# Kernel optimization log

Hardware: AMD Instinct MI355X
Metric: run time of the kernel (lower is better)

Reference implementation:

```python
import jax, jax.numpy as jnp
import numpy as np

GRID_SIZE = 5
SPLINE_ORDER = 3
GRID_LO, GRID_HI = -3.0, 3.0
B, IN_DIM, UNITS, SUB_DIM, NSUB = 4096, 512, 1024, 512, 3


def make_grid(in_features):
    h = (GRID_HI - GRID_LO) / GRID_SIZE
    g = jnp.arange(-SPLINE_ORDER, GRID_SIZE + SPLINE_ORDER + 1, dtype=jnp.float32) * h + GRID_LO
    return jnp.broadcast_to(g, (in_features, g.shape[0]))  # (in, 12)


def b_splines(x, grid):
    # x: (..., in), grid: (in, G) -> (..., in, grid_size + spline_order)
    x = x[..., None]
    bases = ((x >= grid[:, :-1]) & (x < grid[:, 1:])).astype(x.dtype)
    for k in range(1, SPLINE_ORDER + 1):
        left = (x - grid[:, :-(k + 1)]) / (grid[:, k:-1] - grid[:, :-(k + 1)])
        right = (grid[:, k + 1:] - x) / (grid[:, k + 1:] - grid[:, 1:-k])
        bases = left * bases[..., :-1] + right * bases[..., 1:]
    return bases


def setup_inputs() -> dict:
    key = jax.random.key(0)
    ks = jax.random.split(key, 16)
    sw = lambda k, shape, scale: jax.random.normal(k, shape, dtype=jnp.float32) * scale
    inp = {
        'x': sw(ks[0], (B, IN_DIM), 1.0),
        'h0': sw(ks[1], (B, UNITS), 0.1),
        'c0': sw(ks[2], (B, UNITS), 0.1),
        'sub_states': sw(ks[3], (NSUB, B, SUB_DIM), 0.1),
        'kernel': sw(ks[4], (IN_DIM, UNITS * 3), 1.0 / np.sqrt(IN_DIM)),
        'recurrent_kernel': sw(ks[5], (UNITS, UNITS * 3), 1.0 / np.sqrt(UNITS)),
        'bias': jnp.zeros((UNITS * 3,), jnp.float32).at[UNITS:2 * UNITS].set(1.0),
        'sub_kernel_inputs': sw(ks[6], (NSUB, IN_DIM, SUB_DIM), 1.0 / np.sqrt(IN_DIM)),
        'sub_kernel_states': sw(ks[7], (NSUB, SUB_DIM, SUB_DIM), 1.0 / np.sqrt(SUB_DIM)),
        'sub_recurrent_kernel': sw(ks[8], (NSUB, SUB_DIM * 2), 0.5),
        'base_weight': sw(ks[9], (NSUB, SUB_DIM, SUB_DIM), 1.0 / np.sqrt(SUB_DIM)),
        'spline_weight': sw(ks[10], (NSUB, SUB_DIM, SUB_DIM, GRID_SIZE + SPLINE_ORDER), 0.02),
        'spline_scaler': sw(ks[11], (NSUB, SUB_DIM, SUB_DIM), 1.0),
        'aggregated_weight': sw(ks[12], (NSUB * SUB_DIM, UNITS), 1.0 / np.sqrt(NSUB * SUB_DIM)),
        'aggregated_bias': jnp.zeros((UNITS,), jnp.float32),
    }
    return inp


def reference(x, h0, c0, sub_states, kernel, recurrent_kernel, bias,
              sub_kernel_inputs, sub_kernel_states, sub_recurrent_kernel,
              base_weight, spline_weight, spline_scaler,
              aggregated_weight, aggregated_bias):
    grid = make_grid(SUB_DIM)

    # LSTM-style gates: gates = sigmoid(x@W + h@U + b)
    z = x @ kernel + h0 @ recurrent_kernel + bias
    g = jax.nn.sigmoid(z)
    i, f, c_gate = jnp.split(g, 3, axis=-1)
    c_new = f * c0 + i * jnp.tanh(c_gate)

    # Sub-layer inputs: agg[k] = x @ Wx[k] + sub_state[k] @ Wh[k]  -> (k, b, sub_in)
    agg = (jnp.einsum('bi,kis->kbs', x, sub_kernel_inputs)
           + jnp.einsum('kbo,kos->kbs', sub_states, sub_kernel_states))

    # KANLinear: base branch + spline branch (stacked over k sub-layers)
    base_out = jnp.einsum('kbs,kos->kbo', jax.nn.silu(agg), base_weight)
    bases = b_splines(agg, grid)                         # (k, b, sub_in, 8)
    scaled_sw = spline_weight * spline_scaler[..., None]  # (k, out, in, 8)
    spline_out = jnp.einsum('kbic,koic->kbo', bases, scaled_sw)
    sub_out = base_out + spline_out                       # (k, b, sub_out)

    # Recurrent sub-state update
    rk_h = sub_recurrent_kernel[:, None, :SUB_DIM]
    rk_x = sub_recurrent_kernel[:, None, SUB_DIM:]
    new_sub_states = rk_h * sub_out + rk_x * sub_states

    # Output gate from aggregated sub-layer outputs
    agg_flat = jnp.transpose(sub_out, (1, 0, 2)).reshape(x.shape[0], NSUB * SUB_DIM)
    o = jax.nn.sigmoid(agg_flat @ aggregated_weight + aggregated_bias)
    h_new = o * jnp.tanh(c_new)
    return h_new, c_new, new_sub_states
```

## Files before the change

kernel.cpp:

```cpp
#include <hip/hip_runtime.h>

#define B_DIM   4096
#define INF     512
#define UNITS_  1024
#define SUBD    512
#define NSUB_   3
#define NBAS    8
#define G3K     (SUBD * NBAS)

typedef __attribute__((ext_vector_type(8))) short bf16x8_t;
typedef __attribute__((ext_vector_type(4))) float f32x4_t;
typedef unsigned short u16;

__device__ __forceinline__ u16 f2bf(float f) {
    union { float f; unsigned int u; } v; v.f = f;
    unsigned int r = v.u + 0x7fffu + ((v.u >> 16) & 1u);
    return (u16)(r >> 16);
}
__device__ __forceinline__ float bf2f(u16 h) {
    union { unsigned int u; float f; } v; v.u = ((unsigned int)h) << 16;
    return v.f;
}
__device__ __forceinline__ float sigm(float x) { return 1.0f / (1.0f + __expf(-x)); }
__device__ __forceinline__ float tanh_(float x) {
    float e = __expf(2.0f * x);
    return 1.0f - 2.0f / (e + 1.0f);
}

__device__ __forceinline__ void gload_lds16(const void* g, void* l) {
    __builtin_amdgcn_global_load_lds(
        (const __attribute__((address_space(1))) unsigned int*)g,
        (__attribute__((address_space(3))) unsigned int*)l, 16, 0, 0);
}

__global__ void k_f32_to_bf16(const float* __restrict__ in, u16* __restrict__ out, int n4) {
    int i = blockIdx.x * blockDim.x + threadIdx.x;
    if (i >= n4) return;
    float4 v = ((const float4*)in)[i];
    ushort4 r; r.x = f2bf(v.x); r.y = f2bf(v.y); r.z = f2bf(v.z); r.w = f2bf(v.w);
    ((ushort4*)out)[i] = r;
}

__global__ void k_ssw(const float* __restrict__ sw, const float* __restrict__ sc,
                      u16* __restrict__ out, int n4) {
    int i = blockIdx.x * blockDim.x + threadIdx.x;
    if (i >= n4) return;
    float4 v = ((const float4*)sw)[i];
    float s = sc[i >> 1];
    ushort4 r; r.x = f2bf(v.x * s); r.y = f2bf(v.y * s); r.z = f2bf(v.z * s); r.w = f2bf(v.w * s);
    ((ushort4*)out)[i] = r;
}

__global__ void k_tconv(const float* __restrict__ in, u16* __restrict__ out,
                        int R, int C, size_t inStride, size_t outStride) {
    in  += (size_t)blockIdx.z * inStride;
    out += (size_t)blockIdx.z * outStride;
    __shared__ float tile[32][33];
    int c0 = blockIdx.x * 32, r0 = blockIdx.y * 32;
    int tx = threadIdx.x, ty = threadIdx.y;
#pragma unroll
    for (int j = 0; j < 4; ++j)
        tile[ty + j * 8][tx] = in[(size_t)(r0 + ty + j * 8) * C + c0 + tx];
    __syncthreads();
#pragma unroll
    for (int j = 0; j < 4; ++j)
        out[(size_t)(c0 + ty + j * 8) * R + r0 + tx] = f2bf(tile[tx][ty + j * 8]);
}

__global__ void k_cnew(const u16* __restrict__ gbuf, const float* __restrict__ c0,
                       float* __restrict__ c_out, int n4) {
    int i = blockIdx.x * blockDim.x + threadIdx.x;
    if (i >= n4) return;
    int u4 = i * 4;
    int b = u4 >> 10, u = u4 & 1023;
    const u16* gr = gbuf + (size_t)b * 3072 + u;
    ushort4 gi = *(const ushort4*)gr;
    ushort4 gf = *(const ushort4*)(gr + 1024);
    ushort4 gc = *(const ushort4*)(gr + 2048);
    float4 c0v = ((const float4*)c0)[i];
    float4 r;
    r.x = bf2f(gf.x) * c0v.x + bf2f(gi.x) * tanh_(bf2f(gc.x));
    r.y = bf2f(gf.y) * c0v.y + bf2f(gi.y) * tanh_(bf2f(gc.y));
    r.z = bf2f(gf.z) * c0v.z + bf2f(gi.z) * tanh_(bf2f(gc.z));
    r.w = bf2f(gf.w) * c0v.w + bf2f(gi.w) * tanh_(bf2f(gc.w));
    ((float4*)c_out)[i] = r;
}

__global__ void k_bases(const float* __restrict__ agg, u16* __restrict__ bases,
                        u16* __restrict__ silu, int n) {
    for (int i = blockIdx.x * blockDim.x + threadIdx.x; i < n; i += gridDim.x * blockDim.x) {
        float x = agg[i];
        silu[i] = f2bf(x * sigm(x));
        float b[11];
#pragma unroll
        for (int j = 0; j < 11; ++j) {
            float tj  = 1.2f * (float)(j - 3) - 3.0f;
            float tj1 = 1.2f * (float)(j - 2) - 3.0f;
            b[j] = (x >= tj && x < tj1) ? 1.0f : 0.0f;
        }
#pragma unroll
        for (int k = 1; k <= 3; ++k) {
            float inv = 1.0f / (1.2f * (float)k);
#pragma unroll
            for (int j = 0; j < 11; ++j) {
                if (j > 10 - k) break;
                float tj   = 1.2f * (float)(j - 3) - 3.0f;
                float tjk1 = 1.2f * (float)(j + k - 2) - 3.0f;
                b[j] = (x - tj) * inv * b[j] + (tjk1 - x) * inv * b[j + 1];
            }
        }
        bf16x8_t v;
#pragma unroll
        for (int j = 0; j < 8; ++j) v[j] = (short)f2bf(b[j]);
        *(bf16x8_t*)(bases + (size_t)i * 8) = v;
    }
}

struct Seg { const u16* A; const u16* B; int ldA; int ldB; int nkt; };

template<int NS>
__device__ __forceinline__ void gemm_core(const Seg segs[NS], int rowBase, int colBase,
                                          u16* ldsA, u16* ldsB, f32x4_t acc[4][4]) {
    const int t = threadIdx.x;
    const int lane = t & 63, wave = t >> 6;
    const int wR = (wave >> 1) * 64, wC = (wave & 1) * 64;
    const int l15 = lane & 15, lk = (lane >> 4) * 8;
    const int sr = lane >> 3;
    const int scol = (lane & 7) * 8;
#pragma unroll
    for (int s = 0; s < NS; ++s) {
        const u16* Ag = segs[s].A + (size_t)rowBase * segs[s].ldA;
        const u16* Bg = segs[s].B + (size_t)colBase * segs[s].ldB;
        const int ldA = segs[s].ldA, ldB = segs[s].ldB, nkt = segs[s].nkt;
        for (int kt = 0; kt < nkt; ++kt) {
            __syncthreads();
#pragma unroll
            for (int i = 0; i < 4; ++i) {
                int ci = wave * 4 + i;
                int r = ci * 8 + sr;
                gload_lds16(Ag + (size_t)r * ldA + kt * 64 + scol, ldsA + ci * 512);
                gload_lds16(Bg + (size_t)r * ldB + kt * 64 + scol, ldsB + ci * 512);
            }
            __syncthreads();
#pragma unroll
            for (int kk = 0; kk < 2; ++kk) {
                bf16x8_t a[4], b[4];
#pragma unroll
                for (int m = 0; m < 4; ++m)
                    a[m] = *(const bf16x8_t*)(ldsA + (wR + m * 16 + l15) * 64 + kk * 32 + lk);
#pragma unroll
                for (int n = 0; n < 4; ++n)
                    b[n] = *(const bf16x8_t*)(ldsB + (wC + n * 16 + l15) * 64 + kk * 32 + lk);
#pragma unroll
                for (int m = 0; m < 4; ++m)
#pragma unroll
                    for (int n = 0; n < 4; ++n)
                        acc[m][n] = __builtin_amdgcn_mfma_f32_16x16x32_bf16(a[m], b[n], acc[m][n], 0, 0, 0);
            }
        }
    }
}

#define GEMM_PRE()                                                         \
    __shared__ u16 ldsA[128 * 64], ldsB[128 * 64];                         \
    int rowBase = blockIdx.y * 128, colBase = blockIdx.x * 128;            \
    f32x4_t acc[4][4];                                                     \
    _Pragma("unroll") for (int m = 0; m < 4; ++m)                          \
        _Pragma("unroll") for (int n = 0; n < 4; ++n)                      \
            acc[m][n] = (f32x4_t){0.f, 0.f, 0.f, 0.f};

#define EPI_IDX()                                                          \
    const int lane = threadIdx.x & 63, wave = threadIdx.x >> 6;            \
    const int wR = (wave >> 1) * 64, wC = (wave & 1) * 64;                 \
    const int l15 = lane & 15, r4 = (lane >> 4) * 4;

__global__ __launch_bounds__(256) void k_gemm1(const u16* xb, const u16* h0b,
                                               const u16* kT, const u16* rkT,
                                               const float* __restrict__ bias,
                                               u16* __restrict__ gbuf) {
    GEMM_PRE();
    Seg segs[2] = { { xb, kT, INF, INF, INF / 64 },
                    { h0b, rkT, UNITS_, UNITS_, UNITS_ / 64 } };
    gemm_core<2>(segs, rowBase, colBase, ldsA, ldsB, acc);
    EPI_IDX();
#pragma unroll
    for (int m = 0; m < 4; ++m)
#pragma unroll
        for (int n = 0; n < 4; ++n)
#pragma unroll
            for (int j = 0; j < 4; ++j) {
                int row = rowBase + wR + m * 16 + r4 + j;
                int col = colBase + wC + n * 16 + l15;
                gbuf[(size_t)row * 3072 + col] = f2bf(sigm(acc[m][n][j] + bias[col]));
            }
}

__global__ __launch_bounds__(256) void k_gemm2(const u16* xb, const u16* ssb,
                                               const u16* skiT, const u16* sksT,
                                               float* __restrict__ agg) {
    GEMM_PRE();
    int k = blockIdx.z;
    Seg segs[2] = { { xb, skiT + (size_t)k * SUBD * INF, INF, INF, INF / 64 },
                    { ssb + (size_t)k * B_DIM * SUBD, sksT + (size_t)k * SUBD * SUBD, SUBD, SUBD, SUBD / 64 } };
    gemm_core<2>(segs, rowBase, colBase, ldsA, ldsB, acc);
    EPI_IDX();
#pragma unroll
    for (int m = 0; m < 4; ++m)
#pragma unroll
        for (int n = 0; n < 4; ++n)
#pragma unroll
            for (int j = 0; j < 4; ++j) {
                int row = rowBase + wR + m * 16 + r4 + j;
                int col = colBase + wC + n * 16 + l15;
                agg[((size_t)k * B_DIM + row) * SUBD + col] = acc[m][n][j];
            }
}

__global__ __launch_bounds__(256) void k_gemm3(const u16* silu, const u16* bases,
                                               const u16* bwb, const u16* sswb,
                                               const float* __restrict__ srk,
                                               const float* __restrict__ ss,
                                               float* __restrict__ nss_out,
                                               u16* __restrict__ subfl) {
    GEMM_PRE();
    int k = blockIdx.z;
    Seg segs[2] = { { silu + (size_t)k * B_DIM * SUBD, bwb + (size_t)k * SUBD * SUBD, SUBD, SUBD, SUBD / 64 },
                    { bases + (size_t)k * B_DIM * G3K, sswb + (size_t)k * SUBD * G3K, G3K, G3K, G3K / 64 } };
    gemm_core<2>(segs, rowBase, colBase, ldsA, ldsB, acc);
    EPI_IDX();
#pragma unroll
    for (int m = 0; m < 4; ++m)
#pragma unroll
        for (int n = 0; n < 4; ++n)
#pragma unroll
            for (int j = 0; j < 4; ++j) {
                int row = rowBase + wR + m * 16 + r4 + j;
                int col = colBase + wC + n * 16 + l15;
                float so = acc[m][n][j];
                float rh = srk[k * 1024 + col];
                float rx = srk[k * 1024 + 512 + col];
                size_t o = ((size_t)k * B_DIM + row) * SUBD + col;
                nss_out[o] = rh * so + rx * ss[o];
                subfl[(size_t)row * 1536 + k * SUBD + col] = f2bf(so);
            }
}

__global__ __launch_bounds__(256) void k_gemm4(const u16* subfl, const u16* awT,
                                               const float* __restrict__ abias,
                                               const float* __restrict__ c_new,
                                               float* __restrict__ h_out) {
    GEMM_PRE();
    Seg segs[1] = { { subfl, awT, 1536, 1536, 1536 / 64 } };
    gemm_core<1>(segs, rowBase, colBase, ldsA, ldsB, acc);
    EPI_IDX();
#pragma unroll
    for (int m = 0; m < 4; ++m)
#pragma unroll
        for (int n = 0; n < 4; ++n)
#pragma unroll
            for (int j = 0; j < 4; ++j) {
                int row = rowBase + wR + m * 16 + r4 + j;
                int col = colBase + wC + n * 16 + l15;
                float ov = sigm(acc[m][n][j] + abias[col]);
                h_out[(size_t)row * 1024 + col] = ov * tanh_(c_new[(size_t)row * 1024 + col]);
            }
}

extern "C" void kernel_launch(void* const* d_in, const int* in_sizes, int n_in,
                              void* d_out, int out_size, void* d_ws, size_t ws_size,
                              hipStream_t stream) {
    const float* x    = (const float*)d_in[0];
    const float* h0   = (const float*)d_in[1];
    const float* c0   = (const float*)d_in[2];
    const float* ss   = (const float*)d_in[3];
    const float* Wk   = (const float*)d_in[4];
    const float* Wr   = (const float*)d_in[5];
    const float* bias = (const float*)d_in[6];
    const float* ski  = (const float*)d_in[7];
    const float* sks  = (const float*)d_in[8];
    const float* srk  = (const float*)d_in[9];
    const float* bw   = (const float*)d_in[10];
    const float* sw   = (const float*)d_in[11];
    const float* sc   = (const float*)d_in[12];
    const float* aw   = (const float*)d_in[13];
    const float* ab   = (const float*)d_in[14];

    float* out_h   = (float*)d_out;
    float* out_c   = out_h + (size_t)B_DIM * UNITS_;
    float* out_nss = out_c + (size_t)B_DIM * UNITS_;

    char* w = (char*)d_ws;
    auto take = [&](size_t bytes) -> char* {
        char* p = w; w += (bytes + 255) & ~(size_t)255; return p;
    };
    u16*   xb    = (u16*)take((size_t)B_DIM * INF * 2);
    u16*   h0b   = (u16*)take((size_t)B_DIM * UNITS_ * 2);
    u16*   ssb   = (u16*)take((size_t)NSUB_ * B_DIM * SUBD * 2);
    u16*   kT    = (u16*)take((size_t)3072 * INF * 2);
    u16*   rkT   = (u16*)take((size_t)3072 * UNITS_ * 2);
    u16*   skiT  = (u16*)take((size_t)NSUB_ * SUBD * INF * 2);
    u16*   sksT  = (u16*)take((size_t)NSUB_ * SUBD * SUBD * 2);
    u16*   bwb   = (u16*)take((size_t)NSUB_ * SUBD * SUBD * 2);
    u16*   sswb  = (u16*)take((size_t)NSUB_ * SUBD * G3K * 2);
    u16*   awT   = (u16*)take((size_t)UNITS_ * 1536 * 2);
    float* agg   = (float*)take((size_t)NSUB_ * B_DIM * SUBD * 4);
    u16*   siluB = (u16*)take((size_t)NSUB_ * B_DIM * SUBD * 2);
    u16*   subfl = (u16*)take((size_t)B_DIM * 1536 * 2);
    u16*   basesB= (u16*)take((size_t)NSUB_ * B_DIM * G3K * 2);
    u16*   gbuf  = basesB;

    dim3 tb(256);
    k_f32_to_bf16<<<(B_DIM * INF / 4 + 255) / 256, tb, 0, stream>>>(x, xb, B_DIM * INF / 4);
    k_f32_to_bf16<<<(B_DIM * UNITS_ / 4 + 255) / 256, tb, 0, stream>>>(h0, h0b, B_DIM * UNITS_ / 4);
    k_f32_to_bf16<<<(NSUB_ * B_DIM * SUBD / 4 + 255) / 256, tb, 0, stream>>>(ss, ssb, NSUB_ * B_DIM * SUBD / 4);
    k_f32_to_bf16<<<(NSUB_ * SUBD * SUBD / 4 + 255) / 256, tb, 0, stream>>>(bw, bwb, NSUB_ * SUBD * SUBD / 4);
    k_ssw<<<(NSUB_ * SUBD * G3K / 4 + 255) / 256, tb, 0, stream>>>(sw, sc, sswb, NSUB_ * SUBD * G3K / 4);
    dim3 tt(32, 8);
    k_tconv<<<dim3(3072 / 32, INF / 32, 1), tt, 0, stream>>>(Wk, kT, INF, 3072, 0, 0);
    k_tconv<<<dim3(3072 / 32, UNITS_ / 32, 1), tt, 0, stream>>>(Wr, rkT, UNITS_, 3072, 0, 0);
    k_tconv<<<dim3(SUBD / 32, INF / 32, NSUB_), tt, 0, stream>>>(ski, skiT, INF, SUBD,
                                                                 (size_t)INF * SUBD, (size_t)SUBD * INF);
    k_tconv<<<dim3(SUBD / 32, SUBD / 32, NSUB_), tt, 0, stream>>>(sks, sksT, SUBD, SUBD,
                                                                  (size_t)SUBD * SUBD, (size_t)SUBD * SUBD);
    k_tconv<<<dim3(UNITS_ / 32, 1536 / 32, 1), tt, 0, stream>>>(aw, awT, 1536, UNITS_, 0, 0);

    k_gemm1<<<dim3(3072 / 128, B_DIM / 128), tb, 0, stream>>>(xb, h0b, kT, rkT, bias, gbuf);
    k_gemm2<<<dim3(SUBD / 128, B_DIM / 128, NSUB_), tb, 0, stream>>>(xb, ssb, skiT, sksT, agg);
    k_cnew<<<(B_DIM * UNITS_ / 4 + 255) / 256, tb, 0, stream>>>(gbuf, c0, out_c, B_DIM * UNITS_ / 4);

    k_bases<<<4096, tb, 0, stream>>>(agg, basesB, siluB, NSUB_ * B_DIM * SUBD);

    k_gemm3<<<dim3(SUBD / 128, B_DIM / 128, NSUB_), tb, 0, stream>>>(siluB, basesB, bwb, sswb,
                                                                     srk, ss, out_nss, subfl);
    k_gemm4<<<dim3(UNITS_ / 128, B_DIM / 128), tb, 0, stream>>>(subfl, awT, ab, out_c, out_h);
}
```

Before: 521.6 us.

## Split GEMM K-loop across two wave groups with LDS reduction and XCD swizzle

Each GEMM block now has 512 threads split into two 4-wave groups. Each group takes half of the K tiles into its own LDS buffers, and the partial accumulators are summed through LDS before the epilogue. The goal is more waves per tile to hide latency, since launch counts of 256-768 blocks underfill the GPU. k_gemm3 also gets a workgroup-to-XCD swizzle that keeps a chiplet's blocks on contiguous tiles for L2 reuse. In exchange, LDS use doubles to 64KB, which may limit occupancy, and the reduction adds extra syncs and LDS traffic.

```diff
diff --git a/kernel.cpp b/kernel.cpp
--- a/kernel.cpp
+++ b/kernel.cpp
@@ -119,27 +119,31 @@
 struct Seg { const u16* A; const u16* B; int ldA; int ldB; int nkt; };
 
 template<int NS>
-__device__ __forceinline__ void gemm_core(const Seg segs[NS], int rowBase, int colBase,
-                                          u16* ldsA, u16* ldsB, f32x4_t acc[4][4]) {
+__device__ __forceinline__ void gemm_core8(const Seg segs[NS], int rowBase, int colBase,
+                                           u16* smem, f32x4_t acc[4][4]) {
     const int t = threadIdx.x;
     const int lane = t & 63, wave = t >> 6;
-    const int wR = (wave >> 1) * 64, wC = (wave & 1) * 64;
+    const int grp = wave >> 2, w4 = wave & 3;
+    const int wR = (w4 >> 1) * 64, wC = (w4 & 1) * 64;
     const int l15 = lane & 15, lk = (lane >> 4) * 8;
-    const int sr = lane >> 3;
-    const int scol = (lane & 7) * 8;
+    const int sr = lane >> 3, scol = (lane & 7) * 8;
+    u16* lA = smem + grp * 16384;
+    u16* lB = lA + 8192;
 #pragma unroll
     for (int s = 0; s < NS; ++s) {
         const u16* Ag = segs[s].A + (size_t)rowBase * segs[s].ldA;
         const u16* Bg = segs[s].B + (size_t)colBase * segs[s].ldB;
-        const int ldA = segs[s].ldA, ldB = segs[s].ldB, nkt = segs[s].nkt;
-        for (int kt = 0; kt < nkt; ++kt) {
+        const int ldA = segs[s].ldA, ldB = segs[s].ldB;
+        const int khalf = segs[s].nkt >> 1;
+        const int k0 = grp * khalf;
+        for (int kt = 0; kt < khalf; ++kt) {
             __syncthreads();
 #pragma unroll
             for (int i = 0; i < 4; ++i) {
-                int ci = wave * 4 + i;
+                int ci = w4 * 4 + i;
                 int r = ci * 8 + sr;
-                gload_lds16(Ag + (size_t)r * ldA + kt * 64 + scol, ldsA + ci * 512);
-                gload_lds16(Bg + (size_t)r * ldB + kt * 64 + scol, ldsB + ci * 512);
+                gload_lds16(Ag + (size_t)r * ldA + (k0 + kt) * 64 + scol, lA + ci * 512);
+                gload_lds16(Bg + (size_t)r * ldB + (k0 + kt) * 64 + scol, lB + ci * 512);
             }
             __syncthreads();
 #pragma unroll
@@ -147,10 +151,10 @@
                 bf16x8_t a[4], b[4];
 #pragma unroll
                 for (int m = 0; m < 4; ++m)
-                    a[m] = *(const bf16x8_t*)(ldsA + (wR + m * 16 + l15) * 64 + kk * 32 + lk);
+                    a[m] = *(const bf16x8_t*)(lA + (wR + m * 16 + l15) * 64 + kk * 32 + lk);
 #pragma unroll
                 for (int n = 0; n < 4; ++n)
-                    b[n] = *(const bf16x8_t*)(ldsB + (wC + n * 16 + l15) * 64 + kk * 32 + lk);
+                    b[n] = *(const bf16x8_t*)(lB + (wC + n * 16 + l15) * 64 + kk * 32 + lk);
 #pragma unroll
                 for (int m = 0; m < 4; ++m)
 #pragma unroll
@@ -159,111 +163,154 @@
             }
         }
     }
-}
-
-#define GEMM_PRE()                                                         \
-    __shared__ u16 ldsA[128 * 64], ldsB[128 * 64];                         \
-    int rowBase = blockIdx.y * 128, colBase = blockIdx.x * 128;            \
+    __syncthreads();
+    float* red = (float*)smem;
+    const int r4 = (lane >> 4) * 4;
+    if (grp == 1) {
+#pragma unroll
+        for (int m = 0; m < 4; ++m)
+#pragma unroll
+            for (int n = 0; n < 4; ++n)
+#pragma unroll
+                for (int j = 0; j < 4; ++j)
+                    red[(wR + m * 16 + r4 + j) * 128 + wC + n * 16 + l15] = acc[m][n][j];
+    }
+    __syncthreads();
+    if (grp == 0) {
+#pragma unroll
+        for (int m = 0; m < 4; ++m)
+#pragma unroll
+            for (int n = 0; n < 4; ++n)
+#pragma unroll
+                for (int j = 0; j < 4; ++j)
+                    acc[m][n][j] += red[(wR + m * 16 + r4 + j) * 128 + wC + n * 16 + l15];
+    }
+}
+
+template<int NCOL, int NROW, int NWG, bool SWZ>
+__device__ __forceinline__ void decode_wg(int o, int& col, int& row, int& kz) {
+    int wg = o;
+    if (SWZ) {
+        constexpr int q = NWG / 8, r = NWG % 8;
+        int xcd = o & 7, idx = o >> 3;
+        wg = (xcd < r ? xcd * (q + 1) : r * (q + 1) + (xcd - r) * q) + idx;
+    }
+    col = wg % NCOL; int tmp = wg / NCOL; row = tmp % NROW; kz = tmp / NROW;
+}
+
+#define GEMM_PRE8(NCOL, NROW, NWG, SWZ)                                    \
+    __shared__ u16 smem[32768];                                 \
+    int col_, row_, kz_;                                                   \
+    decode_wg<NCOL, NROW, NWG, SWZ>(blockIdx.x, col_, row_, kz_);          \
+    int rowBase = row_ * 128, colBase = col_ * 128;                        \
     f32x4_t acc[4][4];                                                     \
     _Pragma("unroll") for (int m = 0; m < 4; ++m)                          \
         _Pragma("unroll") for (int n = 0; n < 4; ++n)                      \
             acc[m][n] = (f32x4_t){0.f, 0.f, 0.f, 0.f};
 
-#define EPI_IDX()                                                          \
-    const int lane = threadIdx.x & 63, wave = threadIdx.x >> 6;            \
+#define EPI_IDX8()                                                         \
+    const int lane = threadIdx.x & 63, wave = (threadIdx.x >> 6) & 3;      \
     const int wR = (wave >> 1) * 64, wC = (wave & 1) * 64;                 \
     const int l15 = lane & 15, r4 = (lane >> 4) * 4;
 
-__global__ __launch_bounds__(256) void k_gemm1(const u16* xb, const u16* h0b,
+__global__ __launch_bounds__(512) void k_gemm1(const u16* xb, const u16* h0b,
                                                const u16* kT, const u16* rkT,
                                                const float* __restrict__ bias,
                                                u16* __restrict__ gbuf) {
-    GEMM_PRE();
+    GEMM_PRE8(24, 32, 768, false);
     Seg segs[2] = { { xb, kT, INF, INF, INF / 64 },
                     { h0b, rkT, UNITS_, UNITS_, UNITS_ / 64 } };
-    gemm_core<2>(segs, rowBase, colBase, ldsA, ldsB, acc);
-    EPI_IDX();
-#pragma unroll
-    for (int m = 0; m < 4; ++m)
-#pragma unroll
-        for (int n = 0; n < 4; ++n)
-#pragma unroll
-            for (int j = 0; j < 4; ++j) {
-                int row = rowBase + wR + m * 16 + r4 + j;
-                int col = colBase + wC + n * 16 + l15;
-                gbuf[(size_t)row * 3072 + col] = f2bf(sigm(acc[m][n][j] + bias[col]));
-            }
-}
-
-__global__ __launch_bounds__(256) void k_gemm2(const u16* xb, const u16* ssb,
+    gemm_core8<2>(segs, rowBase, colBase, smem, acc);
+    if (threadIdx.x < 256) {
+        EPI_IDX8();
+#pragma unroll
+        for (int m = 0; m < 4; ++m)
+#pragma unroll
+            for (int n = 0; n < 4; ++n)
+#pragma unroll
+                for (int j = 0; j < 4; ++j) {
+                    int row = rowBase + wR + m * 16 + r4 + j;
+                    int col = colBase + wC + n * 16 + l15;
+                    gbuf[(size_t)row * 3072 + col] = f2bf(sigm(acc[m][n][j] + bias[col]));
+                }
+    }
+}
+
+__global__ __launch_bounds__(512) void k_gemm2(const u16* xb, const u16* ssb,
                                                const u16* skiT, const u16* sksT,
                                                float* __restrict__ agg) {
-    GEMM_PRE();
-    int k = blockIdx.z;
+    GEMM_PRE8(4, 32, 384, false);
+    int k = kz_;
     Seg segs[2] = { { xb, skiT + (size_t)k * SUBD * INF, INF, INF, INF / 64 },
                     { ssb + (size_t)k * B_DIM * SUBD, sksT + (size_t)k * SUBD * SUBD, SUBD, SUBD, SUBD / 64 } };
-    gemm_core<2>(segs, rowBase, colBase, ldsA, ldsB, acc);
-    EPI_IDX();
-#pragma unroll
-    for (int m = 0; m < 4; ++m)
-#pragma unroll
-        for (int n = 0; n < 4; ++n)
-#pragma unroll
-            for (int j = 0; j < 4; ++j) {
-                int row = rowBase + wR + m * 16 + r4 + j;
-                int col = colBase + wC + n * 16 + l15;
-                agg[((size_t)k * B_DIM + row) * SUBD + col] = acc[m][n][j];
-            }
-}
-
-__global__ __launch_bounds__(256) void k_gemm3(const u16* silu, const u16* bases,
+    gemm_core8<2>(segs, rowBase, colBase, smem, acc);
+    if (threadIdx.x < 256) {
+        EPI_IDX8();
+#pragma unroll
+        for (int m = 0; m < 4; ++m)
+#pragma unroll
+            for (int n = 0; n < 4; ++n)
+#pragma unroll
+                for (int j = 0; j < 4; ++j) {
+                    int row = rowBase + wR + m * 16 + r4 + j;
+                    int col = colBase + wC + n * 16 + l15;
+                    agg[((size_t)k * B_DIM + row) * SUBD + col] = acc[m][n][j];
+                }
+    }
+}
+
+__global__ __launch_bounds__(512) void k_gemm3(const u16* silu, const u16* bases,
                                                const u16* bwb, const u16* sswb,
                                                const float* __restrict__ srk,
                                                const float* __restrict__ ss,
                                                float* __restrict__ nss_out,
                                                u16* __restrict__ subfl) {
-    GEMM_PRE();
-    int k = blockIdx.z;
+    GEMM_PRE8(4, 32, 384, true);
+    int k = kz_;
     Seg segs[2] = { { silu + (size_t)k * B_DIM * SUBD, bwb + (size_t)k * SUBD * SUBD, SUBD, SUBD, SUBD / 64 },
                     { bases + (size_t)k * B_DIM * G3K, sswb + (size_t)k * SUBD * G3K, G3K, G3K, G3K / 64 } };
-    gemm_core<2>(segs, rowBase, colBase, ldsA, ldsB, acc);
-    EPI_IDX();
-#pragma unroll
-    for (int m = 0; m < 4; ++m)
-#pragma unroll
-        for (int n = 0; n < 4; ++n)
-#pragma unroll
-            for (int j = 0; j < 4; ++j) {
-                int row = rowBase + wR + m * 16 + r4 + j;
-                int col = colBase + wC + n * 16 + l15;
-                float so = acc[m][n][j];
-                float rh = srk[k * 1024 + col];
-                float rx = srk[k * 1024 + 512 + col];
-                size_t o = ((size_t)k * B_DIM + row) * SUBD + col;
-                nss_out[o] = rh * so + rx * ss[o];
-                subfl[(size_t)row * 1536 + k * SUBD + col] = f2bf(so);
-            }
-}
-
-__global__ __launch_bounds__(256) void k_gemm4(const u16* subfl, const u16* awT,
+    gemm_core8<2>(segs, rowBase, colBase, smem, acc);
+    if (threadIdx.x < 256) {
+        EPI_IDX8();
+#pragma unroll
+        for (int m = 0; m < 4; ++m)
+#pragma unroll
+            for (int n = 0; n < 4; ++n)
+#pragma unroll
+                for (int j = 0; j < 4; ++j) {
+                    int row = rowBase + wR + m * 16 + r4 + j;
+                    int col = colBase + wC + n * 16 + l15;
+                    float so = acc[m][n][j];
+                    float rh = srk[k * 1024 + col];
+                    float rx = srk[k * 1024 + 512 + col];
+                    size_t o = ((size_t)k * B_DIM + row) * SUBD + col;
+                    nss_out[o] = rh * so + rx * ss[o];
+                    subfl[(size_t)row * 1536 + k * SUBD + col] = f2bf(so);
+                }
+    }
+}
+
+__global__ __launch_bounds__(512) void k_gemm4(const u16* subfl, const u16* awT,
                                                const float* __restrict__ abias,
                                                const float* __restrict__ c_new,
                                                float* __restrict__ h_out) {
-    GEMM_PRE();
+    GEMM_PRE8(8, 32, 256, false);
     Seg segs[1] = { { subfl, awT, 1536, 1536, 1536 / 64 } };
-    gemm_core<1>(segs, rowBase, colBase, ldsA, ldsB, acc);
-    EPI_IDX();
-#pragma unroll
-    for (int m = 0; m < 4; ++m)
-#pragma unroll
-        for (int n = 0; n < 4; ++n)
-#pragma unroll
-            for (int j = 0; j < 4; ++j) {
-                int row = rowBase + wR + m * 16 + r4 + j;
-                int col = colBase + wC + n * 16 + l15;
-                float ov = sigm(acc[m][n][j] + abias[col]);
-                h_out[(size_t)row * 1024 + col] = ov * tanh_(c_new[(size_t)row * 1024 + col]);
-            }
+    gemm_core8<1>(segs, rowBase, colBase, smem, acc);
+    if (threadIdx.x < 256) {
+        EPI_IDX8();
+#pragma unroll
+        for (int m = 0; m < 4; ++m)
+#pragma unroll
+            for (int n = 0; n < 4; ++n)
+#pragma unroll
+                for (int j = 0; j < 4; ++j) {
+                    int row = rowBase + wR + m * 16 + r4 + j;
+                    int col = colBase + wC + n * 16 + l15;
+                    float ov = sigm(acc[m][n][j] + abias[col]);
+                    h_out[(size_t)row * 1024 + col] = ov * tanh_(c_new[(size_t)row * 1024 + col]);
+                }
+    }
 }
 
 extern "C" void kernel_launch(void* const* d_in, const int* in_sizes, int n_in,
@@ -324,13 +371,12 @@
                                                                   (size_t)SUBD * SUBD, (size_t)SUBD * SUBD);
     k_tconv<<<dim3(UNITS_ / 32, 1536 / 32, 1), tt, 0, stream>>>(aw, awT, 1536, UNITS_, 0, 0);
 
-    k_gemm1<<<dim3(3072 / 128, B_DIM / 128), tb, 0, stream>>>(xb, h0b, kT, rkT, bias, gbuf);
-    k_gemm2<<<dim3(SUBD / 128, B_DIM / 128, NSUB_), tb, 0, stream>>>(xb, ssb, skiT, sksT, agg);
+    k_gemm1<<<768, 512, 0, stream>>>(xb, h0b, kT, rkT, bias, gbuf);
+    k_gemm2<<<384, 512, 0, stream>>>(xb, ssb, skiT, sksT, agg);
     k_cnew<<<(B_DIM * UNITS_ / 4 + 255) / 256, tb, 0, stream>>>(gbuf, c0, out_c, B_DIM * UNITS_ / 4);
 
     k_bases<<<4096, tb, 0, stream>>>(agg, basesB, siluB, NSUB_ * B_DIM * SUBD);
 
-    k_gemm3<<<dim3(SUBD / 128, B_DIM / 128, NSUB_), tb, 0, stream>>>(siluB, basesB, bwb, sswb,
-                                                                     srk, ss, out_nss, subfl);
-    k_gemm4<<<dim3(UNITS_ / 128, B_DIM / 128), tb, 0, stream>>>(subfl, awT, ab, out_c, out_h);
-}
+    k_gemm3<<<384, 512, 0, stream>>>(siluB, basesB, bwb, sswb, srk, ss, out_nss, subfl);
+    k_gemm4<<<256, 512, 0, stream>>>(subfl, awT, ab, out_c, out_h);
+}
```

New measurement: 570.2 us. 9.3% more time.

## Narrow GEMM column tiles to 64 and add XCD-aware block swizzle

Applied to the files above, without the earlier changes.

Templates the GEMM core on tile width so gemm2, gemm3 and gemm4 use 128x64 tiles instead of 128x128, doubling workgroup counts (384 to 768, 256 to 512) so more of the CUs are occupied. All kernels switch to a 1D grid with a decode function. gemm3 also gets an XCD-aware swizzle that groups neighbouring tiles onto the same chiplet to improve L2 reuse of the large bases and spline-weight operands. The cost is that each B-tile is loaded twice as often per A-row and each workgroup does fewer MFMAs per load.

```diff
diff --git a/kernel.cpp b/kernel.cpp
--- a/kernel.cpp
+++ b/kernel.cpp
@@ -118,12 +118,15 @@
 
 struct Seg { const u16* A; const u16* B; int ldA; int ldB; int nkt; };
 
-template<int NS>
-__device__ __forceinline__ void gemm_core(const Seg segs[NS], int rowBase, int colBase,
-                                          u16* ldsA, u16* ldsB, f32x4_t acc[4][4]) {
+template<int NS, int BN>
+__device__ __forceinline__ void gemm_core(const Seg (&segs)[NS], int rowBase, int colBase,
+                                          u16* ldsA, u16* ldsB, f32x4_t (&acc)[4][BN / 32]) {
+    constexpr int NACC = BN / 32;
+    constexpr int NBC  = BN / 8;
+    constexpr int PER  = (16 + NBC) / 4;
     const int t = threadIdx.x;
     const int lane = t & 63, wave = t >> 6;
-    const int wR = (wave >> 1) * 64, wC = (wave & 1) * 64;
+    const int wR = (wave >> 1) * 64, wC = (wave & 1) * (BN / 2);
     const int l15 = lane & 15, lk = (lane >> 4) * 8;
     const int sr = lane >> 3;
     const int scol = (lane & 7) * 8;
@@ -135,54 +138,73 @@
         for (int kt = 0; kt < nkt; ++kt) {
             __syncthreads();
 #pragma unroll
-            for (int i = 0; i < 4; ++i) {
-                int ci = wave * 4 + i;
-                int r = ci * 8 + sr;
-                gload_lds16(Ag + (size_t)r * ldA + kt * 64 + scol, ldsA + ci * 512);
-                gload_lds16(Bg + (size_t)r * ldB + kt * 64 + scol, ldsB + ci * 512);
+            for (int i = 0; i < PER; ++i) {
+                int ci = wave * PER + i;
+                if (ci < 16) {
+                    int r = ci * 8 + sr;
+                    gload_lds16(Ag + (size_t)r * ldA + kt * 64 + scol, ldsA + ci * 512);
+                } else {
+                    int cb = ci - 16;
+                    int r = cb * 8 + sr;
+                    gload_lds16(Bg + (size_t)r * ldB + kt * 64 + scol, ldsB + cb * 512);
+                }
             }
             __syncthreads();
 #pragma unroll
             for (int kk = 0; kk < 2; ++kk) {
-                bf16x8_t a[4], b[4];
+                bf16x8_t a[4], b[NACC];
 #pragma unroll
                 for (int m = 0; m < 4; ++m)
                     a[m] = *(const bf16x8_t*)(ldsA + (wR + m * 16 + l15) * 64 + kk * 32 + lk);
 #pragma unroll
-                for (int n = 0; n < 4; ++n)
+                for (int n = 0; n < NACC; ++n)
                     b[n] = *(const bf16x8_t*)(ldsB + (wC + n * 16 + l15) * 64 + kk * 32 + lk);
 #pragma unroll
                 for (int m = 0; m < 4; ++m)
 #pragma unroll
-                    for (int n = 0; n < 4; ++n)
+                    for (int n = 0; n < NACC; ++n)
                         acc[m][n] = __builtin_amdgcn_mfma_f32_16x16x32_bf16(a[m], b[n], acc[m][n], 0, 0, 0);
             }
         }
     }
 }
 
-#define GEMM_PRE()                                                         \
-    __shared__ u16 ldsA[128 * 64], ldsB[128 * 64];                         \
-    int rowBase = blockIdx.y * 128, colBase = blockIdx.x * 128;            \
-    f32x4_t acc[4][4];                                                     \
+template<int NCOL, int NROW, int NWG, bool SWZ>
+__device__ __forceinline__ void decode_wg(int o, int& col, int& row, int& kz) {
+    int wg = o;
+    if (SWZ) {
+        constexpr int q = NWG / 8, r = NWG % 8;
+        int xcd = o & 7, idx = o >> 3;
+        wg = (xcd < r ? xcd * (q + 1) : r * (q + 1) + (xcd - r) * q) + idx;
+    }
+    col = wg % NCOL; int tmp = wg / NCOL; row = tmp % NROW; kz = tmp / NROW;
+}
+
+#define GEMM_PRE(BN, NCOL, NROW, NWG, SWZ)                                 \
+    __shared__ u16 ldsA[128 * 64];                                         \
+    __shared__ u16 ldsB[BN * 64];                                          \
+    int col_, row_, kz_;                                                   \
+    decode_wg<NCOL, NROW, NWG, SWZ>(blockIdx.x, col_, row_, kz_);          \
+    int rowBase = row_ * 128, colBase = col_ * BN;                         \
+    f32x4_t acc[4][BN / 32];                                               \
     _Pragma("unroll") for (int m = 0; m < 4; ++m)                          \
-        _Pragma("unroll") for (int n = 0; n < 4; ++n)                      \
+        _Pragma("unroll") for (int n = 0; n < BN / 32; ++n)                \
             acc[m][n] = (f32x4_t){0.f, 0.f, 0.f, 0.f};
 
-#define EPI_IDX()                                                          \
+#define EPI_IDX(BN)                                                        \
     const int lane = threadIdx.x & 63, wave = threadIdx.x >> 6;            \
-    const int wR = (wave >> 1) * 64, wC = (wave & 1) * 64;                 \
+    const int wR = (wave >> 1) * 64, wC = (wave & 1) * (BN / 2);           \
     const int l15 = lane & 15, r4 = (lane >> 4) * 4;
 
 __global__ __launch_bounds__(256) void k_gemm1(const u16* xb, const u16* h0b,
                                                const u16* kT, const u16* rkT,
                                                const float* __restrict__ bias,
                                                u16* __restrict__ gbuf) {
-    GEMM_PRE();
+    GEMM_PRE(128, 24, 32, 768, false);
     Seg segs[2] = { { xb, kT, INF, INF, INF / 64 },
                     { h0b, rkT, UNITS_, UNITS_, UNITS_ / 64 } };
-    gemm_core<2>(segs, rowBase, colBase, ldsA, ldsB, acc);
-    EPI_IDX();
+    gemm_core<2, 128>(segs, rowBase, colBase, ldsA, ldsB, acc);
+    EPI_IDX(128);
 #pragma unroll
     for (int m = 0; m < 4; ++m)
 #pragma unroll
@@ -198,16 +220,16 @@
 __global__ __launch_bounds__(256) void k_gemm2(const u16* xb, const u16* ssb,
                                                const u16* skiT, const u16* sksT,
                                                float* __restrict__ agg) {
-    GEMM_PRE();
-    int k = blockIdx.z;
+    GEMM_PRE(64, 8, 32, 768, false);
+    int k = kz_;
     Seg segs[2] = { { xb, skiT + (size_t)k * SUBD * INF, INF, INF, INF / 64 },
                     { ssb + (size_t)k * B_DIM * SUBD, sksT + (size_t)k * SUBD * SUBD, SUBD, SUBD, SUBD / 64 } };
-    gemm_core<2>(segs, rowBase, colBase, ldsA, ldsB, acc);
-    EPI_IDX();
+    gemm_core<2, 64>(segs, rowBase, colBase, ldsA, ldsB, acc);
+    EPI_IDX(64);
 #pragma unroll
     for (int m = 0; m < 4; ++m)
 #pragma unroll
-        for (int n = 0; n < 4; ++n)
+        for (int n = 0; n < 2; ++n)
 #pragma unroll
             for (int j = 0; j < 4; ++j) {
                 int row = rowBase + wR + m * 16 + r4 + j;
@@ -222,16 +244,16 @@
                                                const float* __restrict__ ss,
                                                float* __restrict__ nss_out,
                                                u16* __restrict__ subfl) {
-    GEMM_PRE();
-    int k = blockIdx.z;
+    GEMM_PRE(64, 8, 32, 768, true);
+    int k = kz_;
     Seg segs[2] = { { silu + (size_t)k * B_DIM * SUBD, bwb + (size_t)k * SUBD * SUBD, SUBD, SUBD, SUBD / 64 },
                     { bases + (size_t)k * B_DIM * G3K, sswb + (size_t)k * SUBD * G3K, G3K, G3K, G3K / 64 } };
-    gemm_core<2>(segs, rowBase, colBase, ldsA, ldsB, acc);
-    EPI_IDX();
+    gemm_core<2, 64>(segs, rowBase, colBase, ldsA, ldsB, acc);
+    EPI_IDX(64);
 #pragma unroll
     for (int m = 0; m < 4; ++m)
 #pragma unroll
-        for (int n = 0; n < 4; ++n)
+        for (int n = 0; n < 2; ++n)
 #pragma unroll
             for (int j = 0; j < 4; ++j) {
                 int row = rowBase + wR + m * 16 + r4 + j;
@@ -249,14 +271,14 @@
                                                const float* __restrict__ abias,
                                                const float* __restrict__ c_new,
                                                float* __restrict__ h_out) {
-    GEMM_PRE();
+    GEMM_PRE(64, 16, 32, 512, false);
     Seg segs[1] = { { subfl, awT, 1536, 1536, 1536 / 64 } };
-    gemm_core<1>(segs, rowBase, colBase, ldsA, ldsB, acc);
-    EPI_IDX();
+    gemm_core<1, 64>(segs, rowBase, colBase, ldsA, ldsB, acc);
+    EPI_IDX(64);
 #pragma unroll
     for (int m = 0; m < 4; ++m)
 #pragma unroll
-        for (int n = 0; n < 4; ++n)
+        for (int n = 0; n < 2; ++n)
 #pragma unroll
             for (int j = 0; j < 4; ++j) {
                 int row = rowBase + wR + m * 16 + r4 + j;
@@ -324,13 +346,12 @@
                                                                   (size_t)SUBD * SUBD, (size_t)SUBD * SUBD);
     k_tconv<<<dim3(UNITS_ / 32, 1536 / 32, 1), tt, 0, stream>>>(aw, awT, 1536, UNITS_, 0, 0);
 
-    k_gemm1<<<dim3(3072 / 128, B_DIM / 128), tb, 0, stream>>>(xb, h0b, kT, rkT, bias, gbuf);
-    k_gemm2<<<dim3(SUBD / 128, B_DIM / 128, NSUB_), tb, 0, stream>>>(xb, ssb, skiT, sksT, agg);
+    k_gemm1<<<768, tb, 0, stream>>>(xb, h0b, kT, rkT, bias, gbuf);
+    k_gemm2<<<768, tb, 0, stream>>>(xb, ssb, skiT, sksT, agg);
     k_cnew<<<(B_DIM * UNITS_ / 4 + 255) / 256, tb, 0, stream>>>(gbuf, c0, out_c, B_DIM * UNITS_ / 4);
 
     k_bases<<<4096, tb, 0, stream>>>(agg, basesB, siluB, NSUB_ * B_DIM * SUBD);
 
-    k_gemm3<<<dim3(SUBD / 128, B_DIM / 128, NSUB_), tb, 0, stream>>>(siluB, basesB, bwb, sswb,
-                                                                     srk, ss, out_nss, subfl);
-    k_gemm4<<<dim3(UNITS_ / 128, B_DIM / 128), tb, 0, stream>>>(subfl, awT, ab, out_c, out_h);
-}
+    k_gemm3<<<768, tb, 0, stream>>>(siluB, basesB, bwb, sswb, srk, ss, out_nss, subfl);
+    k_gemm4<<<512, tb, 0, stream>>>(subfl, awT, ab, out_c, out_h);
+}
```

Measured after the change: 500.9 us. 1.04x faster.
